# Performance work log

Measured on AMD Instinct MI355X. Metric: run time of the kernel, lower is better.

Reference implementation:

```python
import jax, jax.numpy as jnp
import numpy as np

B, T, C, HS = 512, 256, 256, 64

def setup_inputs() -> dict:
    key = jax.random.key(0)
    kx, kq, kk, kv = jax.random.split(key, 4)
    x = jax.random.normal(kx, (B, T, C), dtype=jnp.float32)
    # nn.Linear(n_embd, head_size, bias=False): store as [in, out] for x @ W
    Wq = jax.random.normal(kq, (C, HS), dtype=jnp.float32) * (C ** -0.5)
    Wk = jax.random.normal(kk, (C, HS), dtype=jnp.float32) * (C ** -0.5)
    Wv = jax.random.normal(kv, (C, HS), dtype=jnp.float32) * (C ** -0.5)
    return {"x": x, "Wq": Wq, "Wk": Wk, "Wv": Wv}

def reference(x, Wq, Wk, Wv):
    # self-attention path (key_input/value_input are None)
    q = x @ Wq  # [B, T, HS]
    k = x @ Wk
    v = x @ Wv
    # NOTE: original scales by C**-0.5 (full embed dim), not head_size**-0.5
    wei = jnp.einsum('bqd,bkd->bqk', q, k) * (C ** -0.5)  # [B, T, T]
    Tq = x.shape[1]
    causal = jnp.tril(jnp.ones((Tq, Tq), dtype=bool))
    wei = jnp.where(causal, wei, -jnp.inf)
    wei = jax.nn.softmax(wei, axis=-1)
    # dropout p=0 -> identity
    out = wei @ v  # [B, T, HS]
    return out
```

## Files before the change

### kernel.cpp

```cpp
#include <hip/hip_runtime.h>
#include <hip/hip_bf16.h>
#include <cstdint>
#include <cmath>

#define B_ 512
#define T_ 256
#define C_ 256
#define HS_ 64

typedef short bf16x8 __attribute__((ext_vector_type(8)));
typedef float f32x4 __attribute__((ext_vector_type(4)));

static __device__ __forceinline__ unsigned short f2bf(float f) {
    union { float f; unsigned int u; } v; v.f = f;
    unsigned int r = v.u + 0x7fffu + ((v.u >> 16) & 1u);
    return (unsigned short)(r >> 16);
}

static __device__ __forceinline__ uint2 pack4(f32x4 a) {
    uint2 r;
    r.x = (unsigned)f2bf(a[0]) | ((unsigned)f2bf(a[1]) << 16);
    r.y = (unsigned)f2bf(a[2]) | ((unsigned)f2bf(a[3]) << 16);
    return r;
}

__global__ void wt_kernel(const float* __restrict__ Wq, const float* __restrict__ Wk,
                          const float* __restrict__ Wv, unsigned short* __restrict__ WTf) {
    int idx = blockIdx.x * 256 + threadIdx.x;
    if (idx >= 96 * 64) return;
    int fb = idx >> 6;
    int l = idx & 63;
    int ws = fb >> 5;
    int rem = fb & 31;
    int f = rem >> 3;
    int kap = rem & 7;
    const float* W = (ws == 0) ? Wq : ((ws == 1) ? Wk : Wv);
    unsigned short o[8];
#pragma unroll
    for (int j = 0; j < 8; ++j) {
        int k = kap * 32 + (l >> 4) * 8 + j;
        int n = f * 16 + (l & 15);
        o[j] = f2bf(W[k * HS_ + n]);
    }
    *(ulonglong2*)(WTf + (size_t)idx * 8) = *(ulonglong2*)o;
}

__global__ __launch_bounds__(512, 2)
void fused_kernel(const float* __restrict__ x, const unsigned short* __restrict__ WTf,
                  float* __restrict__ out) {
    __shared__ __align__(16) char smem[163840];
    unsigned short* Qs  = (unsigned short*)(smem);
    unsigned short* Ks  = (unsigned short*)(smem + 32768);
    unsigned short* Vts = (unsigned short*)(smem + 65536);
    char* xbuf = smem + 98304;

    const int tid = threadIdx.x;
    const int w = tid >> 6, l = tid & 63, ln = l & 15, lg = l >> 4;
    const int b = blockIdx.x;
    const float* xb = x + (size_t)b * (T_ * C_);
    const int fidbase = 3 * (w >> 1);
    const int Tb = (w & 1) * 4;
    const float scale = 0.0625f;

#pragma unroll
    for (int r = 0; r < 12; ++r)
        __builtin_amdgcn_global_load_lds(
            (const __attribute__((address_space(1))) void*)((const char*)WTf + r * 8192 + tid * 16),
            (__attribute__((address_space(3))) void*)(smem + r * 8192 + tid * 16), 16, 0, 0);

    float4 st[16];
#pragma unroll
    for (int i = 0; i < 16; ++i)
        st[i] = *(const float4*)(xb + (size_t)(i * 512 + tid) * 4);

    uint2 h0[12], h1[12];

#define DS_WRITE_SLAB() do { \
    _Pragma("unroll") \
    for (int i_ = 0; i_ < 16; ++i_) { \
        const int fidx_ = i_ * 512 + tid, row_ = fidx_ >> 6, c4_ = (fidx_ & 63) * 4; \
        ushort4 hh_; \
        hh_.x = f2bf(st[i_].x); hh_.y = f2bf(st[i_].y); \
        hh_.z = f2bf(st[i_].z); hh_.w = f2bf(st[i_].w); \
        *(ushort4*)(xbuf + row_ * 512 + ((c4_ * 2) ^ ((row_ & 7) << 4))) = hh_; \
    } \
} while (0)

#define SLAB_COMPUTE(H) do { \
    f32x4 acc_[12]; \
    _Pragma("unroll") \
    for (int k_ = 0; k_ < 12; ++k_) acc_[k_] = (f32x4){0.f, 0.f, 0.f, 0.f}; \
    _Pragma("unroll") \
    for (int kap_ = 0; kap_ < 8; ++kap_) { \
        bf16x8 bfr_[3]; \
        _Pragma("unroll") \
        for (int j_ = 0; j_ < 3; ++j_) \
            bfr_[j_] = *(const bf16x8*)(smem + (size_t)((fidbase + j_) * 8 + kap_) * 1024 + l * 16); \
        _Pragma("unroll") \
        for (int tt_ = 0; tt_ < 4; ++tt_) { \
            const int R_ = (Tb + tt_) * 16 + ln; \
            bf16x8 afr_ = *(const bf16x8*)(xbuf + R_ * 512 \
                           + ((kap_ * 64 + lg * 16) ^ ((R_ & 7) << 4))); \
            _Pragma("unroll") \
            for (int j_ = 0; j_ < 3; ++j_) \
                acc_[tt_ * 3 + j_] = __builtin_amdgcn_mfma_f32_16x16x32_bf16( \
                    bfr_[j_], afr_, acc_[tt_ * 3 + j_], 0, 0, 0); \
        } \
    } \
    _Pragma("unroll") \
    for (int k_ = 0; k_ < 12; ++k_) H[k_] = pack4(acc_[k_]); \
} while (0)

    DS_WRITE_SLAB();
    __syncthreads();
#pragma unroll
    for (int i = 0; i < 16; ++i)
        st[i] = *(const float4*)(xb + 32768 + (size_t)(i * 512 + tid) * 4);
    SLAB_COMPUTE(h0);
    __syncthreads();

    DS_WRITE_SLAB();
    __syncthreads();
    SLAB_COMPUTE(h1);
    __syncthreads();

#pragma unroll
    for (int s = 0; s < 2; ++s) {
#pragma unroll
        for (int tt = 0; tt < 4; ++tt)
#pragma unroll
            for (int j = 0; j < 3; ++j) {
                uint2 hv = s ? h1[tt * 3 + j] : h0[tt * 3 + j];
                const int token = s * 128 + (Tb + tt) * 16 + ln;
                const int fid = fidbase + j, f = fid & 3;
                if (fid < 8) {
                    unsigned short* base_ = (fid < 4) ? Qs : Ks;
                    *(uint2*)((char*)base_ + token * 128
                              + ((f * 32 + lg * 8) ^ ((token & 7) << 4))) = hv;
                } else {
                    unsigned short v4[4] = {
                        (unsigned short)(hv.x & 0xffff), (unsigned short)(hv.x >> 16),
                        (unsigned short)(hv.y & 0xffff), (unsigned short)(hv.y >> 16)};
#pragma unroll
                    for (int i = 0; i < 4; ++i) {
                        const int vr = f * 16 + lg * 4 + i;
                        *(unsigned short*)((char*)Vts + vr * 512
                              + ((token * 2) ^ ((vr & 7) << 4))) = v4[i];
                    }
                }
            }
    }
    __syncthreads();

    unsigned short* Pl = (unsigned short*)(xbuf + w * 1280);
    float* outb = out + (size_t)b * (T_ * HS_);

#pragma unroll
    for (int pass = 0; pass < 2; ++pass) {
        const int g = pass ? (15 - w) : w;
        const int r0 = g * 16;
        const int qrow = r0 + ln;

        bf16x8 qa[2];
#pragma unroll
        for (int kk = 0; kk < 2; ++kk)
            qa[kk] = *(const bf16x8*)((char*)Qs + (r0 + ln) * 128
                       + ((kk * 64 + lg * 16) ^ ((ln & 7) << 4)));

        float m = -INFINITY, lsum = 0.f;
        f32x4 o[4];
#pragma unroll
        for (int f = 0; f < 4; ++f) o[f] = (f32x4){0.f, 0.f, 0.f, 0.f};

        const int nkt = (g >> 1) + 1;
        for (int kt = 0; kt < nkt; ++kt) {
            const int n0 = kt * 32;

            f32x4 s2[2];
#pragma unroll
            for (int h = 0; h < 2; ++h) {
                const int key = n0 + 16 * h + ln;
                bf16x8 kb0 = *(const bf16x8*)((char*)Ks + key * 128
                               + ((lg * 16) ^ ((key & 7) << 4)));
                bf16x8 kb1 = *(const bf16x8*)((char*)Ks + key * 128
                               + ((64 + lg * 16) ^ ((key & 7) << 4)));
                f32x4 z = (f32x4){0.f, 0.f, 0.f, 0.f};
                z = __builtin_amdgcn_mfma_f32_16x16x32_bf16(kb0, qa[0], z, 0, 0, 0);
                s2[h] = __builtin_amdgcn_mfma_f32_16x16x32_bf16(kb1, qa[1], z, 0, 0, 0);
            }

            float sm[2][4];
#pragma unroll
            for (int h = 0; h < 2; ++h)
#pragma unroll
                for (int r = 0; r < 4; ++r) {
                    const int key = n0 + 16 * h + lg * 4 + r;
                    float v = s2[h][r] * scale;
                    sm[h][r] = (qrow >= key) ? v : -INFINITY;
                }

            float tmax = fmaxf(fmaxf(fmaxf(sm[0][0], sm[0][1]), fmaxf(sm[0][2], sm[0][3])),
                               fmaxf(fmaxf(sm[1][0], sm[1][1]), fmaxf(sm[1][2], sm[1][3])));
            tmax = fmaxf(tmax, __shfl_xor(tmax, 16, 64));
            tmax = fmaxf(tmax, __shfl_xor(tmax, 32, 64));

            const float mn = fmaxf(m, tmax);
            const float fac = __expf(m - mn);
            float p[2][4];
            float rs = 0.f;
#pragma unroll
            for (int h = 0; h < 2; ++h)
#pragma unroll
                for (int r = 0; r < 4; ++r) {
                    p[h][r] = __expf(sm[h][r] - mn);
                    rs += p[h][r];
                }
            rs += __shfl_xor(rs, 16, 64);
            rs += __shfl_xor(rs, 32, 64);
            lsum = lsum * fac + rs;
            m = mn;
#pragma unroll
            for (int f = 0; f < 4; ++f) o[f] *= fac;

#pragma unroll
            for (int h = 0; h < 2; ++h)
#pragma unroll
                for (int rp = 0; rp < 2; ++rp) {
                    unsigned pk = (unsigned)f2bf(p[h][2 * rp])
                                | ((unsigned)f2bf(p[h][2 * rp + 1]) << 16);
                    *(unsigned*)(Pl + ln * 40 + 16 * h + lg * 4 + 2 * rp) = pk;
                }

            bf16x8 pa = *(const bf16x8*)(Pl + ln * 40 + lg * 8);

#pragma unroll
            for (int f = 0; f < 4; ++f) {
                const int vr = f * 16 + ln;
                bf16x8 vb = *(const bf16x8*)((char*)Vts + vr * 512
                              + ((n0 * 2 + lg * 16) ^ ((ln & 7) << 4)));
                o[f] = __builtin_amdgcn_mfma_f32_16x16x32_bf16(vb, pa, o[f], 0, 0, 0);
            }
        }

        const float inv = 1.f / lsum;
#pragma unroll
        for (int f = 0; f < 4; ++f) {
            float4 sv;
            sv.x = o[f][0] * inv; sv.y = o[f][1] * inv;
            sv.z = o[f][2] * inv; sv.w = o[f][3] * inv;
            *(float4*)(outb + (size_t)qrow * HS_ + f * 16 + lg * 4) = sv;
        }
    }
}

extern "C" void kernel_launch(void* const* d_in, const int* in_sizes, int n_in,
                              void* d_out, int out_size, void* d_ws, size_t ws_size,
                              hipStream_t stream) {
    const float* x  = (const float*)d_in[0];
    const float* Wq = (const float*)d_in[1];
    const float* Wk = (const float*)d_in[2];
    const float* Wv = (const float*)d_in[3];
    float* out = (float*)d_out;

    unsigned short* WTf = (unsigned short*)d_ws;

    wt_kernel<<<24, 256, 0, stream>>>(Wq, Wk, Wv, WTf);
    fused_kernel<<<B_, 512, 0, stream>>>(x, WTf, out);
}
```

Baseline: 61.26 us.

## Stream x in small slabs and keep Q in registers to halve LDS

Restructures the projection phase so x is streamed in eight 32-row slabs with a small register prefetch. Weights are read straight from global/L2 instead of staged in LDS, and Q stays in registers and goes through LDS only briefly to redistribute fragments. This halves LDS use, which is meant to allow more resident blocks per CU. It also skips the online-softmax rescale when no lane's running max grows. The cost is more barriers per slab, repeated global weight fetches, and a more serialized projection loop.

```diff
diff --git a/kernel.cpp b/kernel.cpp
--- a/kernel.cpp
+++ b/kernel.cpp
@@ -45,39 +45,32 @@
     *(ulonglong2*)(WTf + (size_t)idx * 8) = *(ulonglong2*)o;
 }
 
-__global__ __launch_bounds__(512, 2)
+__global__ __launch_bounds__(512, 4)
 void fused_kernel(const float* __restrict__ x, const unsigned short* __restrict__ WTf,
                   float* __restrict__ out) {
-    __shared__ __align__(16) char smem[163840];
-    unsigned short* Qs  = (unsigned short*)(smem);
-    unsigned short* Ks  = (unsigned short*)(smem + 32768);
-    unsigned short* Vts = (unsigned short*)(smem + 65536);
-    char* xbuf = smem + 98304;
+    __shared__ __align__(16) char smem[81920];
+    unsigned short* Ks  = (unsigned short*)(smem);
+    unsigned short* Vts = (unsigned short*)(smem + 32768);
+    char* xbuf = smem + 65536;
 
     const int tid = threadIdx.x;
     const int w = tid >> 6, l = tid & 63, ln = l & 15, lg = l >> 4;
     const int b = blockIdx.x;
     const float* xb = x + (size_t)b * (T_ * C_);
-    const int fidbase = 3 * (w >> 1);
-    const int Tb = (w & 1) * 4;
+    const int qt = w >> 2, qf = w & 3;
     const float scale = 0.0625f;
 
-#pragma unroll
-    for (int r = 0; r < 12; ++r)
-        __builtin_amdgcn_global_load_lds(
-            (const __attribute__((address_space(1))) void*)((const char*)WTf + r * 8192 + tid * 16),
-            (__attribute__((address_space(3))) void*)(smem + r * 8192 + tid * 16), 16, 0, 0);
-
-    float4 st[16];
-#pragma unroll
-    for (int i = 0; i < 16; ++i)
-        st[i] = *(const float4*)(xb + (size_t)(i * 512 + tid) * 4);
-
-    uint2 h0[12], h1[12];
+    float4 st[4];
+
+#define LOADX(S) do { \
+    _Pragma("unroll") \
+    for (int i_ = 0; i_ < 4; ++i_) \
+        st[i_] = *(const float4*)(xb + (S) * 8192 + (size_t)(i_ * 512 + tid) * 4); \
+} while (0)
 
 #define DS_WRITE_SLAB() do { \
     _Pragma("unroll") \
-    for (int i_ = 0; i_ < 16; ++i_) { \
+    for (int i_ = 0; i_ < 4; ++i_) { \
         const int fidx_ = i_ * 512 + tid, row_ = fidx_ >> 6, c4_ = (fidx_ & 63) * 4; \
         ushort4 hh_; \
         hh_.x = f2bf(st[i_].x); hh_.y = f2bf(st[i_].y); \
@@ -86,69 +79,82 @@
     } \
 } while (0)
 
-#define SLAB_COMPUTE(H) do { \
-    f32x4 acc_[12]; \
-    _Pragma("unroll") \
-    for (int k_ = 0; k_ < 12; ++k_) acc_[k_] = (f32x4){0.f, 0.f, 0.f, 0.f}; \
-    _Pragma("unroll") \
-    for (int kap_ = 0; kap_ < 8; ++kap_) { \
-        bf16x8 bfr_[3]; \
-        _Pragma("unroll") \
-        for (int j_ = 0; j_ < 3; ++j_) \
-            bfr_[j_] = *(const bf16x8*)(smem + (size_t)((fidbase + j_) * 8 + kap_) * 1024 + l * 16); \
-        _Pragma("unroll") \
-        for (int tt_ = 0; tt_ < 4; ++tt_) { \
-            const int R_ = (Tb + tt_) * 16 + ln; \
-            bf16x8 afr_ = *(const bf16x8*)(xbuf + R_ * 512 \
-                           + ((kap_ * 64 + lg * 16) ^ ((R_ & 7) << 4))); \
-            _Pragma("unroll") \
-            for (int j_ = 0; j_ < 3; ++j_) \
-                acc_[tt_ * 3 + j_] = __builtin_amdgcn_mfma_f32_16x16x32_bf16( \
-                    bfr_[j_], afr_, acc_[tt_ * 3 + j_], 0, 0, 0); \
-        } \
-    } \
-    _Pragma("unroll") \
-    for (int k_ = 0; k_ < 12; ++k_) H[k_] = pack4(acc_[k_]); \
-} while (0)
-
-    DS_WRITE_SLAB();
-    __syncthreads();
-#pragma unroll
-    for (int i = 0; i < 16; ++i)
-        st[i] = *(const float4*)(xb + 32768 + (size_t)(i * 512 + tid) * 4);
-    SLAB_COMPUTE(h0);
-    __syncthreads();
-
-    DS_WRITE_SLAB();
-    __syncthreads();
-    SLAB_COMPUTE(h1);
-    __syncthreads();
-
-#pragma unroll
-    for (int s = 0; s < 2; ++s) {
-#pragma unroll
-        for (int tt = 0; tt < 4; ++tt)
-#pragma unroll
-            for (int j = 0; j < 3; ++j) {
-                uint2 hv = s ? h1[tt * 3 + j] : h0[tt * 3 + j];
-                const int token = s * 128 + (Tb + tt) * 16 + ln;
-                const int fid = fidbase + j, f = fid & 3;
-                if (fid < 8) {
-                    unsigned short* base_ = (fid < 4) ? Qs : Ks;
-                    *(uint2*)((char*)base_ + token * 128
-                              + ((f * 32 + lg * 8) ^ ((token & 7) << 4))) = hv;
-                } else {
-                    unsigned short v4[4] = {
-                        (unsigned short)(hv.x & 0xffff), (unsigned short)(hv.x >> 16),
-                        (unsigned short)(hv.y & 0xffff), (unsigned short)(hv.y >> 16)};
-#pragma unroll
-                    for (int i = 0; i < 4; ++i) {
-                        const int vr = f * 16 + lg * 4 + i;
-                        *(unsigned short*)((char*)Vts + vr * 512
-                              + ((token * 2) ^ ((vr & 7) << 4))) = v4[i];
-                    }
-                }
-            }
+    uint2 hqQ[8];
+
+    LOADX(0);
+#pragma unroll
+    for (int s = 0; s < 8; ++s) {
+        DS_WRITE_SLAB();
+        __syncthreads();
+        if (s < 7) LOADX(s + 1);
+
+        f32x4 aq   = (f32x4){0.f, 0.f, 0.f, 0.f};
+        f32x4 akv0 = (f32x4){0.f, 0.f, 0.f, 0.f};
+        f32x4 akv1 = (f32x4){0.f, 0.f, 0.f, 0.f};
+#pragma unroll
+        for (int kap = 0; kap < 8; ++kap) {
+            bf16x8 bq  = *(const bf16x8*)(WTf + ((size_t)(qf * 8 + kap) * 64 + l) * 8);
+            bf16x8 bkv = *(const bf16x8*)(WTf + ((size_t)((4 + w) * 8 + kap) * 64 + l) * 8);
+            bf16x8 a0 = *(const bf16x8*)(xbuf + ln * 512
+                          + ((kap * 64 + lg * 16) ^ ((ln & 7) << 4)));
+            const int R1 = 16 + ln;
+            bf16x8 a1 = *(const bf16x8*)(xbuf + R1 * 512
+                          + ((kap * 64 + lg * 16) ^ ((R1 & 7) << 4)));
+            akv0 = __builtin_amdgcn_mfma_f32_16x16x32_bf16(bkv, a0, akv0, 0, 0, 0);
+            akv1 = __builtin_amdgcn_mfma_f32_16x16x32_bf16(bkv, a1, akv1, 0, 0, 0);
+            aq   = __builtin_amdgcn_mfma_f32_16x16x32_bf16(bq, qt ? a1 : a0, aq, 0, 0, 0);
+        }
+        hqQ[s] = pack4(aq);
+
+        if (w < 4) {
+#pragma unroll
+            for (int tt = 0; tt < 2; ++tt) {
+                const int token = s * 32 + tt * 16 + ln;
+                uint2 hv = pack4(tt ? akv1 : akv0);
+                *(uint2*)((char*)Ks + token * 128
+                          + ((w * 32 + lg * 8) ^ ((token & 7) << 4))) = hv;
+            }
+        } else {
+#pragma unroll
+            for (int tt = 0; tt < 2; ++tt) {
+                const int token = s * 32 + tt * 16 + ln;
+                f32x4 av = tt ? akv1 : akv0;
+#pragma unroll
+                for (int i = 0; i < 4; ++i) {
+                    const int vr = (w - 4) * 16 + lg * 4 + i;
+                    *(unsigned short*)((char*)Vts + vr * 512
+                          + ((token * 2) ^ ((vr & 7) << 4))) = f2bf(av[i]);
+                }
+            }
+        }
+        __syncthreads();
+    }
+
+    bf16x8 qa0[2], qa1[2];
+#pragma unroll
+    for (int s = 0; s < 4; ++s) {
+        const int row = s * 32 + qt * 16 + ln;
+        *(uint2*)(xbuf + row * 128 + ((qf * 32 + lg * 8) ^ ((row & 7) << 4))) = hqQ[s];
+    }
+    __syncthreads();
+#pragma unroll
+    for (int kk = 0; kk < 2; ++kk) {
+        const int row = w * 16 + ln;
+        qa0[kk] = *(const bf16x8*)(xbuf + row * 128
+                    + ((kk * 64 + lg * 16) ^ ((row & 7) << 4)));
+    }
+    __syncthreads();
+#pragma unroll
+    for (int s = 4; s < 8; ++s) {
+        const int row = (s - 4) * 32 + qt * 16 + ln;
+        *(uint2*)(xbuf + row * 128 + ((qf * 32 + lg * 8) ^ ((row & 7) << 4))) = hqQ[s];
+    }
+    __syncthreads();
+#pragma unroll
+    for (int kk = 0; kk < 2; ++kk) {
+        const int row = (7 - w) * 16 + ln;
+        qa1[kk] = *(const bf16x8*)(xbuf + row * 128
+                    + ((kk * 64 + lg * 16) ^ ((row & 7) << 4)));
     }
     __syncthreads();
 
@@ -160,12 +166,6 @@
         const int g = pass ? (15 - w) : w;
         const int r0 = g * 16;
         const int qrow = r0 + ln;
-
-        bf16x8 qa[2];
-#pragma unroll
-        for (int kk = 0; kk < 2; ++kk)
-            qa[kk] = *(const bf16x8*)((char*)Qs + (r0 + ln) * 128
-                       + ((kk * 64 + lg * 16) ^ ((ln & 7) << 4)));
 
         float m = -INFINITY, lsum = 0.f;
         f32x4 o[4];
@@ -185,8 +185,8 @@
                 bf16x8 kb1 = *(const bf16x8*)((char*)Ks + key * 128
                                + ((64 + lg * 16) ^ ((key & 7) << 4)));
                 f32x4 z = (f32x4){0.f, 0.f, 0.f, 0.f};
-                z = __builtin_amdgcn_mfma_f32_16x16x32_bf16(kb0, qa[0], z, 0, 0, 0);
-                s2[h] = __builtin_amdgcn_mfma_f32_16x16x32_bf16(kb1, qa[1], z, 0, 0, 0);
+                z = __builtin_amdgcn_mfma_f32_16x16x32_bf16(kb0, pass ? qa1[0] : qa0[0], z, 0, 0, 0);
+                s2[h] = __builtin_amdgcn_mfma_f32_16x16x32_bf16(kb1, pass ? qa1[1] : qa0[1], z, 0, 0, 0);
             }
 
             float sm[2][4];
@@ -204,23 +204,27 @@
             tmax = fmaxf(tmax, __shfl_xor(tmax, 16, 64));
             tmax = fmaxf(tmax, __shfl_xor(tmax, 32, 64));
 
-            const float mn = fmaxf(m, tmax);
-            const float fac = __expf(m - mn);
+            if (!__all(tmax <= m)) {
+                const float mn = fmaxf(m, tmax);
+                const float fac = __expf(m - mn);
+                lsum *= fac;
+                m = mn;
+#pragma unroll
+                for (int f = 0; f < 4; ++f) o[f] *= fac;
+            }
+
             float p[2][4];
             float rs = 0.f;
 #pragma unroll
             for (int h = 0; h < 2; ++h)
 #pragma unroll
                 for (int r = 0; r < 4; ++r) {
-                    p[h][r] = __expf(sm[h][r] - mn);
+                    p[h][r] = __expf(sm[h][r] - m);
                     rs += p[h][r];
                 }
             rs += __shfl_xor(rs, 16, 64);
             rs += __shfl_xor(rs, 32, 64);
-            lsum = lsum * fac + rs;
-            m = mn;
-#pragma unroll
-            for (int f = 0; f < 4; ++f) o[f] *= fac;
+            lsum += rs;
 
 #pragma unroll
             for (int h = 0; h < 2; ++h)
@@ -237,7 +241,7 @@
             for (int f = 0; f < 4; ++f) {
                 const int vr = f * 16 + ln;
                 bf16x8 vb = *(const bf16x8*)((char*)Vts + vr * 512
-                              + ((n0 * 2 + lg * 16) ^ ((ln & 7) << 4)));
+                              + ((n0 * 2 + lg * 16) ^ ((vr & 7) << 4)));
                 o[f] = __builtin_amdgcn_mfma_f32_16x16x32_bf16(vb, pa, o[f], 0, 0, 0);
             }
         }
```

Result: slower. 64.43 us (+5.2%).
